# Optimization experiments

Hardware: AMD Instinct MI355X
Metric: run time of the kernel (lower is better)

The kernel has to match this reference:

```python
import jax, jax.numpy as jnp
import numpy as np
from jax import lax

B, C, T_IN = 512, 22, 1001   # input width includes the subject-id column
K, KS, P = 40, 25, 100       # num_kernels, kernel_size, pool_size
S, NOUT = 9, 4               # num_subjects, n_outputs
BN_EPS = 1e-5


def setup_inputs() -> dict:
    key = jax.random.key(0)
    ks = jax.random.split(key, 6)
    x = jax.random.normal(ks[0], (B, C, T_IN), dtype=jnp.float32)
    # subject ids in 1..9 encoded as id*1e6 at x[:, 0, -1] (as in the torch module)
    sid = jax.random.randint(ks[1], (B,), 1, S + 1)
    x = x.at[:, 0, -1].set(sid.astype(jnp.float32) * 1e6)
    W = 0.05 * jax.random.normal(ks[2], (S, K, C, KS), dtype=jnp.float32)
    b = 0.05 * jax.random.normal(ks[3], (S, K), dtype=jnp.float32)
    gamma = jnp.ones((K,), dtype=jnp.float32)
    beta = jnp.zeros((K,), dtype=jnp.float32)
    fc_in = K * ((T_IN - 1 - KS + 1) // P)  # 40 * 9 = 360
    fc_w = 0.05 * jax.random.normal(ks[4], (NOUT, fc_in), dtype=jnp.float32)
    fc_b = jnp.zeros((NOUT,), dtype=jnp.float32)
    return {"x": x, "W": W, "b": b, "gamma": gamma, "beta": beta,
            "fc_w": fc_w, "fc_b": fc_b}


def reference(x, W, b, gamma, beta, fc_w, fc_b):
    # decode per-sample subject routing id (0-based into stacked weights)
    sid = (x[:, 0, -1] / 1e6).astype(jnp.int32) - 1        # [B]
    xs = x[:, :, :-1]                                      # [B, C, T]
    Wg = W[sid]                                            # [B, K, C, KS] gathered expert weights
    bg = b[sid]                                            # [B, K]

    # per-sample 1D valid conv with its own expert weights (batched via vmap)
    def conv1(xi, wi):  # xi: [C, T], wi: [K, C, KS]
        return lax.conv_general_dilated(xi[None], wi, (1,), 'VALID',
                                        dimension_numbers=('NCH', 'OIH', 'NCH'))[0]

    y = jax.vmap(conv1)(xs, Wg) + bg[:, :, None]           # [B, K, To]
    y = jax.nn.elu(y)

    # BatchNorm2d in training mode: batch statistics over (B, spatial), biased var
    mean = y.mean(axis=(0, 2))
    var = y.var(axis=(0, 2))
    y = (y - mean[None, :, None]) * (gamma / jnp.sqrt(var + BN_EPS))[None, :, None] \
        + beta[None, :, None]

    # AvgPool over non-overlapping windows of size P (stride = P, floor)
    To = y.shape[-1]
    nw = To // P
    y = y[..., : nw * P].reshape(y.shape[0], K, nw, P).mean(axis=-1)  # [B, K, nw]

    y = y.reshape(y.shape[0], -1)          # [B, K*nw]; dropout is identity in eval
    return y @ fc_w.T + fc_b               # [B, NOUT]
```

## Files before the change

kernel.cpp:

```cpp
#include <hip/hip_runtime.h>
#include <hip/hip_bf16.h>

#define B_ 512
#define C_ 22
#define TIN 1001
#define K_ 40
#define KS_ 25
#define TO 976
#define P_ 100
#define NW 9
#define NOUT 4
#define FCIN 360

#define QROWS 280
#define XT_BYTES (QROWS * 64)
#define RED_OFF XT_BYTES
#define RED_BYTES (K_ * 4 * 2 * 4)
#define LDS_TOTAL (RED_OFF + RED_BYTES)
#define NBLKQ 2048
#define NPAD 48
#define WB_ELEM_S (KS_ * NPAD * 32)

typedef __attribute__((ext_vector_type(8))) short bf16x8;
typedef __attribute__((ext_vector_type(4))) float f32x4;
typedef __attribute__((ext_vector_type(4))) int i32x4;

__device__ __forceinline__ float waveReduceSum(float v) {
#pragma unroll
  for (int m = 32; m >= 1; m >>= 1) v += __shfl_xor(v, m, 64);
  return v;
}

__device__ __forceinline__ unsigned short f2bf(float f) {
  __hip_bfloat16 h = __float2bfloat16(f);
  return *reinterpret_cast<unsigned short*>(&h);
}

__global__ __launch_bounds__(192) void wconv_kernel(const float* __restrict__ W,
                                                    unsigned short* __restrict__ WBg) {
  const int s = blockIdx.x / KS_;
  const int j = blockIdx.x % KS_;
  const int n = threadIdx.x >> 2;
  const int q = threadIdx.x & 3;
  union {
    unsigned short u[8];
    i32x4 v;
  } pk;
#pragma unroll
  for (int e = 0; e < 8; ++e) {
    const int c = q * 8 + e;
    float v = 0.f;
    if (n < K_ && c < C_) v = W[(((size_t)s * K_ + n) * C_ + c) * KS_ + j];
    pk.u[e] = f2bf(v);
  }
  *(i32x4*)(WBg + ((size_t)(s * KS_ + j) * NPAD + n) * 32 + q * 8) = pk.v;
}

#define MFMA12(A, Bv)                                                          \
  do {                                                                         \
    _Pragma("unroll") for (int nt_ = 0; nt_ < 3; ++nt_) {                      \
      _Pragma("unroll") for (int m_ = 0; m_ < 4; ++m_) {                       \
        acc[m_][nt_] =                                                         \
            __builtin_amdgcn_mfma_f32_16x16x32_bf16(A[m_], Bv[nt_], acc[m_][nt_], 0, 0, 0); \
      }                                                                        \
    }                                                                          \
  } while (0)

#define LDA(J, A)                                                              \
  do {                                                                         \
    const int tl_ = tbl + (J);                                                 \
    const char* ap_ = sm + tl_ * 64 + ((lg ^ ((tl_ >> 1) & 3)) << 4);          \
    _Pragma("unroll") for (int m_ = 0; m_ < 4; ++m_) {                         \
      A[m_] = *(const bf16x8*)(ap_ + m_ * 1024);                               \
    }                                                                          \
  } while (0)

#define LDB(J, Bv)                                                             \
  do {                                                                         \
    const unsigned short* bp_ = WBs + (J) * 1536;                              \
    _Pragma("unroll") for (int nt_ = 0; nt_ < 3; ++nt_) {                      \
      Bv[nt_] = *(const bf16x8*)(bp_ + nt_ * 512);                             \
    }                                                                          \
  } while (0)

__global__ __launch_bounds__(256, 3) void conv_kernel(
    const float* __restrict__ x, const unsigned short* __restrict__ WBg,
    const float* __restrict__ bias, float* __restrict__ pooled,
    float* __restrict__ part_sum, float* __restrict__ part_sq) {
  extern __shared__ __align__(16) char sm[];
  const int blk = blockIdx.x;
  const int b = blk >> 2;
  const int p = blk & 3;
  const int rbg = p * 256;
  const int tid = threadIdx.x;

  int s = (int)rintf(x[(size_t)b * (C_ * TIN) + (TIN - 1)] * 1e-6f) - 1;
  s = __builtin_amdgcn_readfirstlane(min(max(s, 0), 8));

  {
    const float* xb = x + (size_t)b * (C_ * TIN);
    for (int task = tid; task < 4 * QROWS; task += 256) {
      const int q = task / QROWS;
      const int tr = task - q * QROWS;
      const int lq = q ^ ((tr >> 1) & 3);
      const int tg = rbg + tr;
      union {
        unsigned short u[8];
        i32x4 v;
      } pk;
#pragma unroll
      for (int e = 0; e < 8; ++e) {
        const int c = lq * 8 + e;
        float v = 0.f;
        if (c < C_ && tg < TIN - 1) v = xb[c * TIN + tg];
        pk.u[e] = f2bf(v);
      }
      *(i32x4*)(sm + tr * 64 + q * 16) = pk.v;
    }
  }
  __syncthreads();

  const int lane = tid & 63;
  const int wv = tid >> 6;
  const int l15 = lane & 15;
  const int lg = lane >> 4;
  const int tbl = wv * 64 + l15;

  const unsigned short* WBs = WBg + (size_t)s * WB_ELEM_S + (l15 * 32 + lg * 8);

  f32x4 acc[4][3];
#pragma unroll
  for (int m = 0; m < 4; ++m)
#pragma unroll
    for (int nt = 0; nt < 3; ++nt) acc[m][nt] = (f32x4){0.f, 0.f, 0.f, 0.f};

  bf16x8 Aa[2][4];
  bf16x8 Bb[4][3];

  LDA(0, Aa[0]);
#pragma unroll
  for (int jj = 0; jj < 3; ++jj) LDB(jj, Bb[jj]);

#pragma unroll
  for (int j = 0; j <= 24; ++j) {
    if (j < 24) LDA(j + 1, Aa[(j + 1) & 1]);
    if (j + 3 <= 24) LDB(j + 3, Bb[(j + 3) & 3]);
    __builtin_amdgcn_s_setprio(1);
    MFMA12(Aa[j & 1], Bb[j & 3]);
    __builtin_amdgcn_s_setprio(0);
  }

  float bv[3];
#pragma unroll
  for (int nt = 0; nt < 3; ++nt) {
    const int k = nt * 16 + l15;
    bv[nt] = bias[s * K_ + (k < K_ ? k : 0)];
  }
  const int wbase = rbg / P_;
  const int base100 = wbase * P_;
  float sY[3] = {0.f, 0.f, 0.f}, sY2[3] = {0.f, 0.f, 0.f};
  float pw[4][3];
#pragma unroll
  for (int w4 = 0; w4 < 4; ++w4)
#pragma unroll
    for (int nt = 0; nt < 3; ++nt) pw[w4][nt] = 0.f;

#pragma unroll
  for (int m = 0; m < 4; ++m) {
#pragma unroll
    for (int i = 0; i < 4; ++i) {
      const int t = rbg + wv * 64 + m * 16 + lg * 4 + i;
      const bool valid = (t < TO);
      const bool pool = (t < NW * P_);
      const int d = t - base100;
#pragma unroll
      for (int nt = 0; nt < 3; ++nt) {
        const float v = acc[m][nt][i] + bv[nt];
        const float y = v > 0.f ? v : expm1f(v);
        if (valid) {
          sY[nt] += y;
          sY2[nt] += y * y;
          if (pool) {
            if (d < P_)
              pw[0][nt] += y;
            else if (d < 2 * P_)
              pw[1][nt] += y;
            else if (d < 3 * P_)
              pw[2][nt] += y;
            else
              pw[3][nt] += y;
          }
        }
      }
    }
  }

  float* red = (float*)(sm + RED_OFF);
#pragma unroll
  for (int nt = 0; nt < 3; ++nt) {
#pragma unroll
    for (int r = 16; r <= 32; r <<= 1) {
      pw[0][nt] += __shfl_xor(pw[0][nt], r, 64);
      pw[1][nt] += __shfl_xor(pw[1][nt], r, 64);
      pw[2][nt] += __shfl_xor(pw[2][nt], r, 64);
      pw[3][nt] += __shfl_xor(pw[3][nt], r, 64);
      sY[nt] += __shfl_xor(sY[nt], r, 64);
      sY2[nt] += __shfl_xor(sY2[nt], r, 64);
    }
    const int k = nt * 16 + l15;
    if (lane < 16 && k < K_) {
      float* pb = pooled + (size_t)b * FCIN + k * NW;
#pragma unroll
      for (int w4 = 0; w4 < 4; ++w4) {
        const int wg = wbase + w4;
        if (wg <= NW - 1 && pw[w4][nt] != 0.f) atomicAdd(&pb[wg], pw[w4][nt]);
      }
      red[k * 4 + wv] = sY[nt];
      red[K_ * 4 + k * 4 + wv] = sY2[nt];
    }
  }
  __syncthreads();
  if (tid < K_) {
    float a = 0.f, q = 0.f;
#pragma unroll
    for (int i = 0; i < 4; ++i) {
      a += red[tid * 4 + i];
      q += red[K_ * 4 + tid * 4 + i];
    }
    part_sum[(size_t)tid * NBLKQ + blk] = a;
    part_sq[(size_t)tid * NBLKQ + blk] = q;
  }
}

__global__ __launch_bounds__(256) void stats_kernel(
    const float* __restrict__ part_sum, const float* __restrict__ part_sq,
    const float* __restrict__ gamma, const float* __restrict__ beta,
    float* __restrict__ ss) {
  const int k = blockIdx.x;
  float s = 0.f, q = 0.f;
  for (int i = threadIdx.x; i < NBLKQ; i += 256) {
    s += part_sum[(size_t)k * NBLKQ + i];
    q += part_sq[(size_t)k * NBLKQ + i];
  }
  s = waveReduceSum(s);
  q = waveReduceSum(q);
  __shared__ float ls[4], lq[4];
  const int wave = threadIdx.x >> 6, lane = threadIdx.x & 63;
  if (lane == 0) {
    ls[wave] = s;
    lq[wave] = q;
  }
  __syncthreads();
  if (threadIdx.x == 0) {
    const float S = ls[0] + ls[1] + ls[2] + ls[3];
    const float Q = lq[0] + lq[1] + lq[2] + lq[3];
    const float N = (float)B_ * (float)TO;
    const float mean = S / N;
    const float var = Q / N - mean * mean;
    const float sc = gamma[k] / sqrtf(var + 1e-5f);
    ss[k] = sc;
    ss[K_ + k] = beta[k] - mean * sc;
  }
}

__global__ __launch_bounds__(256) void fc_kernel(
    const float* __restrict__ pooled, const float* __restrict__ ss,
    const float* __restrict__ fc_w, const float* __restrict__ fc_b,
    float* __restrict__ out) {
  const int bb = blockIdx.x;
  const int n = threadIdx.x >> 6;
  const int lane = threadIdx.x & 63;
  float acc = 0.f;
  for (int i = lane; i < FCIN; i += 64) {
    const int k = i / NW;
    const float y = pooled[(size_t)bb * FCIN + i] * (1.f / (float)P_) * ss[k] + ss[K_ + k];
    acc = fmaf(y, fc_w[n * FCIN + i], acc);
  }
  acc = waveReduceSum(acc);
  if (lane == 0) out[bb * NOUT + n] = acc + fc_b[n];
}

extern "C" void kernel_launch(void* const* d_in, const int* in_sizes, int n_in,
                              void* d_out, int out_size, void* d_ws, size_t ws_size,
                              hipStream_t stream) {
  const float* x = (const float*)d_in[0];
  const float* W = (const float*)d_in[1];
  const float* bias = (const float*)d_in[2];
  const float* gamma = (const float*)d_in[3];
  const float* beta = (const float*)d_in[4];
  const float* fc_w = (const float*)d_in[5];
  const float* fc_b = (const float*)d_in[6];
  float* out = (float*)d_out;

  char* ws = (char*)d_ws;
  float* pooled = (float*)ws;
  float* part_sum = (float*)(ws + 737280);
  float* part_sq = (float*)(ws + 1064960);
  unsigned short* WBg = (unsigned short*)(ws + 1392640);
  float* ss = (float*)(ws + 2083840);

  hipFuncSetAttribute((const void*)conv_kernel,
                      hipFuncAttributeMaxDynamicSharedMemorySize, LDS_TOTAL);

  hipMemsetAsync(pooled, 0, 737280, stream);
  wconv_kernel<<<9 * KS_, 192, 0, stream>>>(W, WBg);
  conv_kernel<<<NBLKQ, 256, LDS_TOTAL, stream>>>(x, WBg, bias, pooled, part_sum, part_sq);
  stats_kernel<<<K_, 256, 0, stream>>>(part_sum, part_sq, gamma, beta, ss);
  fc_kernel<<<B_, 256, 0, stream>>>(pooled, ss, fc_w, fc_b, out);
}
```

Baseline: 107.5 us.

## Pre-transpose input to bf16 in separate kernel and stage via global_load_lds

Adds an xpose_kernel that converts x once into a swizzled bf16 time-major layout in workspace. The conv kernel then fills LDS with direct global-to-LDS 16-byte loads instead of doing strided fp32 loads and conversion per block, which removes overlapping-halo recomputation and the strided gather cost. It also shrinks the B-operand prefetch depth from 3 to 2 to raise occupancy to 4 blocks per SIMD, and uses fast __expf in ELU. The trade-off is an extra kernel launch and an extra round trip of roughly 36 MB through global memory, plus reduced ELU precision.

```diff
diff --git a/kernel.cpp b/kernel.cpp
--- a/kernel.cpp
+++ b/kernel.cpp
@@ -12,9 +12,10 @@
 #define NOUT 4
 #define FCIN 360
 
-#define QROWS 280
-#define XT_BYTES (QROWS * 64)
-#define RED_OFF XT_BYTES
+#define XTROWS 1088
+#define SROWS 320
+#define STG_BYTES (SROWS * 64)
+#define RED_OFF STG_BYTES
 #define RED_BYTES (K_ * 4 * 2 * 4)
 #define LDS_TOTAL (RED_OFF + RED_BYTES)
 #define NBLKQ 2048
@@ -34,6 +35,12 @@
 __device__ __forceinline__ unsigned short f2bf(float f) {
   __hip_bfloat16 h = __float2bfloat16(f);
   return *reinterpret_cast<unsigned short*>(&h);
+}
+
+__device__ __forceinline__ void gll16(const void* g, void* l) {
+  __builtin_amdgcn_global_load_lds(
+      (const __attribute__((address_space(1))) unsigned int*)g,
+      (__attribute__((address_space(3))) unsigned int*)l, 16, 0, 0);
 }
 
 __global__ __launch_bounds__(192) void wconv_kernel(const float* __restrict__ W,
@@ -56,6 +63,32 @@
   *(i32x4*)(WBg + ((size_t)(s * KS_ + j) * NPAD + n) * 32 + q * 8) = pk.v;
 }
 
+__global__ __launch_bounds__(256) void xpose_kernel(const float* __restrict__ x,
+                                                    unsigned short* __restrict__ XTg) {
+  const int b = blockIdx.x;
+  const float* xb = x + (size_t)b * (C_ * TIN);
+  unsigned short* xt = XTg + (size_t)b * XTROWS * 32;
+#pragma unroll 1
+  for (int r = 0; r < 17; ++r) {
+    const int task = threadIdx.x + r * 256;
+    const int q = task / XTROWS;
+    const int tr = task - q * XTROWS;
+    const int lq = q ^ ((tr >> 1) & 3);
+    union {
+      unsigned short u[8];
+      i32x4 v;
+    } pk;
+#pragma unroll
+    for (int e = 0; e < 8; ++e) {
+      const int c = lq * 8 + e;
+      float v = 0.f;
+      if (c < C_ && tr < TIN - 1) v = xb[c * TIN + tr];
+      pk.u[e] = f2bf(v);
+    }
+    *(i32x4*)(xt + (size_t)tr * 32 + q * 8) = pk.v;
+  }
+}
+
 #define MFMA12(A, Bv)                                                          \
   do {                                                                         \
     _Pragma("unroll") for (int nt_ = 0; nt_ < 3; ++nt_) {                      \
@@ -83,10 +116,11 @@
     }                                                                          \
   } while (0)
 
-__global__ __launch_bounds__(256, 3) void conv_kernel(
-    const float* __restrict__ x, const unsigned short* __restrict__ WBg,
-    const float* __restrict__ bias, float* __restrict__ pooled,
-    float* __restrict__ part_sum, float* __restrict__ part_sq) {
+__global__ __launch_bounds__(256, 4) void conv_kernel(
+    const unsigned short* __restrict__ XTg, const unsigned short* __restrict__ WBg,
+    const float* __restrict__ x, const float* __restrict__ bias,
+    float* __restrict__ pooled, float* __restrict__ part_sum,
+    float* __restrict__ part_sq) {
   extern __shared__ __align__(16) char sm[];
   const int blk = blockIdx.x;
   const int b = blk >> 2;
@@ -98,24 +132,11 @@
   s = __builtin_amdgcn_readfirstlane(min(max(s, 0), 8));
 
   {
-    const float* xb = x + (size_t)b * (C_ * TIN);
-    for (int task = tid; task < 4 * QROWS; task += 256) {
-      const int q = task / QROWS;
-      const int tr = task - q * QROWS;
-      const int lq = q ^ ((tr >> 1) & 3);
-      const int tg = rbg + tr;
-      union {
-        unsigned short u[8];
-        i32x4 v;
-      } pk;
-#pragma unroll
-      for (int e = 0; e < 8; ++e) {
-        const int c = lq * 8 + e;
-        float v = 0.f;
-        if (c < C_ && tg < TIN - 1) v = xb[c * TIN + tg];
-        pk.u[e] = f2bf(v);
-      }
-      *(i32x4*)(sm + tr * 64 + q * 16) = pk.v;
+    const char* src = (const char*)XTg + ((size_t)b * XTROWS + rbg) * 64;
+#pragma unroll
+    for (int r = 0; r < 5; ++r) {
+      const int i = tid + r * 256;
+      gll16(src + i * 16, sm + i * 16);
     }
   }
   __syncthreads();
@@ -135,18 +156,18 @@
     for (int nt = 0; nt < 3; ++nt) acc[m][nt] = (f32x4){0.f, 0.f, 0.f, 0.f};
 
   bf16x8 Aa[2][4];
-  bf16x8 Bb[4][3];
+  bf16x8 Bb[3][3];
 
   LDA(0, Aa[0]);
-#pragma unroll
-  for (int jj = 0; jj < 3; ++jj) LDB(jj, Bb[jj]);
+  LDB(0, Bb[0]);
+  LDB(1, Bb[1]);
 
 #pragma unroll
   for (int j = 0; j <= 24; ++j) {
     if (j < 24) LDA(j + 1, Aa[(j + 1) & 1]);
-    if (j + 3 <= 24) LDB(j + 3, Bb[(j + 3) & 3]);
+    if (j + 2 <= 24) LDB(j + 2, Bb[(j + 2) % 3]);
     __builtin_amdgcn_s_setprio(1);
-    MFMA12(Aa[j & 1], Bb[j & 3]);
+    MFMA12(Aa[j & 1], Bb[j % 3]);
     __builtin_amdgcn_s_setprio(0);
   }
 
@@ -176,10 +197,10 @@
 #pragma unroll
       for (int nt = 0; nt < 3; ++nt) {
         const float v = acc[m][nt][i] + bv[nt];
-        const float y = v > 0.f ? v : expm1f(v);
+        const float y = v > 0.f ? v : (__expf(v) - 1.f);
         if (valid) {
           sY[nt] += y;
-          sY2[nt] += y * y;
+          sY2[nt] = fmaf(y, y, sY2[nt]);
           if (pool) {
             if (d < P_)
               pw[0][nt] += y;
@@ -298,13 +319,16 @@
   float* part_sq = (float*)(ws + 1064960);
   unsigned short* WBg = (unsigned short*)(ws + 1392640);
   float* ss = (float*)(ws + 2083840);
-
-  hipFuncSetAttribute((const void*)conv_kernel,
-                      hipFuncAttributeMaxDynamicSharedMemorySize, LDS_TOTAL);
-
-  hipMemsetAsync(pooled, 0, 737280, stream);
+  unsigned short* XTg = (unsigned short*)(ws + 2084160);
+
+  (void)hipFuncSetAttribute((const void*)conv_kernel,
+                            hipFuncAttributeMaxDynamicSharedMemorySize, LDS_TOTAL);
+
+  (void)hipMemsetAsync(pooled, 0, 737280, stream);
   wconv_kernel<<<9 * KS_, 192, 0, stream>>>(W, WBg);
-  conv_kernel<<<NBLKQ, 256, LDS_TOTAL, stream>>>(x, WBg, bias, pooled, part_sum, part_sq);
+  xpose_kernel<<<B_, 256, 0, stream>>>(x, XTg);
+  conv_kernel<<<NBLKQ, 256, LDS_TOTAL, stream>>>(XTg, WBg, x, bias, pooled,
+                                                 part_sum, part_sq);
   stats_kernel<<<K_, 256, 0, stream>>>(part_sum, part_sq, gamma, beta, ss);
   fc_kernel<<<B_, 256, 0, stream>>>(pooled, ss, fc_w, fc_b, out);
 }
```

After: 127.2 us. 1.18x slower.
